# Optimization experiments

Measured on AMD Instinct MI355X. Metric: run time of the kernel, lower is better.

## Reference

```python
import jax, jax.numpy as jnp
import numpy as np

B, S, D_IN, D_H, D_OUT = 8, 4096, 512, 1024, 512


def setup_inputs() -> dict:
    key = jax.random.key(0)
    ks = jax.random.split(key, 7)
    # scale weights by 1/sqrt(fan_in) so activations stay O(1) through the ReLU stack
    return {
        "query": jax.random.normal(ks[0], (B, S, D_IN), dtype=jnp.float32),
        "W0": jax.random.normal(ks[1], (B, D_H, D_IN), dtype=jnp.float32) * (D_IN ** -0.5),
        "b0": jax.random.normal(ks[2], (B, D_H), dtype=jnp.float32) * 0.02,
        "W1": jax.random.normal(ks[3], (B, D_H, D_H), dtype=jnp.float32) * (D_H ** -0.5),
        "b1": jax.random.normal(ks[4], (B, D_H), dtype=jnp.float32) * 0.02,
        "W2": jax.random.normal(ks[5], (B, D_OUT, D_H), dtype=jnp.float32) * (D_H ** -0.5),
        "b2": jax.random.normal(ks[6], (B, D_OUT), dtype=jnp.float32) * 0.02,
    }


def reference(query, W0, b0, W1, b1, W2, b2):
    # Original loops over (seq, batch) issuing F.linear per sample with per-batch
    # weights; this is exactly a batched GEMM over the batch axis.
    # F.linear(x, w, b) = x @ w.T + b, with w[b] of shape [out, in].
    h = jax.nn.relu(jnp.einsum('bsd,bhd->bsh', query, W0) + b0[:, None, :])  # [B,S,H]
    h = jax.nn.relu(jnp.einsum('bsh,bgh->bsg', h, W1) + b1[:, None, :])      # [B,S,H]
    out = jnp.einsum('bsg,bog->bso', h, W2) + b2[:, None, :]                 # [B,S,O]
    return out
```

## Files before the change

kernel.cpp:

```cpp
#include <hip/hip_runtime.h>


typedef _Float16 f16x8 __attribute__((ext_vector_type(8)));
typedef _Float16 f16x4 __attribute__((ext_vector_type(4)));
typedef float    f32x4 __attribute__((ext_vector_type(4)));

__device__ __forceinline__ void stage16(const void* g, void* l) {
    __builtin_amdgcn_global_load_lds(
        (const __attribute__((address_space(1))) unsigned int*)g,
        (__attribute__((address_space(3))) unsigned int*)l,
        16, 0, 0);
}

__device__ __forceinline__ void cast_seg(const float* __restrict__ s,
                                         _Float16* __restrict__ d, int n4) {
    const int stride = gridDim.x * 256;
    for (int i = blockIdx.x * 256 + threadIdx.x; i < n4; i += stride) {
        float4 f = reinterpret_cast<const float4*>(s)[i];
        f16x4 o;
        o[0] = (_Float16)f.x; o[1] = (_Float16)f.y;
        o[2] = (_Float16)f.z; o[3] = (_Float16)f.w;
        reinterpret_cast<f16x4*>(d)[i] = o;
    }
}

__global__ __launch_bounds__(256) void cast_all(
    const float* s0, _Float16* d0, int n0,
    const float* s1, _Float16* d1, int n1,
    const float* s2, _Float16* d2, int n2,
    const float* s3, _Float16* d3, int n3) {
    cast_seg(s0, d0, n0);
    cast_seg(s1, d1, n1);
    cast_seg(s2, d2, n2);
    cast_seg(s3, d3, n3);
}

template <bool RELU, bool OUT_F16>
__global__ __launch_bounds__(512, 2) void gemm_pipe(
    const _Float16* __restrict__ A, const _Float16* __restrict__ W,
    const float* __restrict__ bias, void* __restrict__ Outv,
    int M, int N, int K) {
    constexpr int BM = 256, BN = 256, BK = 32;
    constexpr int DEPTH = 4;
    __shared__ __align__(16) _Float16 As[DEPTH][BM * BK];
    __shared__ __align__(16) _Float16 Bs[DEPTH][BN * BK];

    const int tid  = threadIdx.x;
    const int lane = tid & 63;
    const int rowl = lane & 15;
    const int q8   = (lane >> 4) * 8;
    const int w    = tid >> 6;
    const int wm   = (w >> 2) * 128;
    const int wn   = (w & 3) * 64;

    const int bm = blockIdx.x, bn = blockIdx.y, b = blockIdx.z;

    const int c0 = tid, c1 = tid + 512;
    const int ar0 = c0 >> 2, ak0 = (c0 & 3) * 8;
    const int ar1 = c1 >> 2, ak1 = (c1 & 3) * 8;

    const char* Ab = (const char*)(A + (size_t)b * M * K + (size_t)(bm * BM) * K);
    const char* Wb = (const char*)(W + (size_t)b * N * K + (size_t)(bn * BN) * K);
    size_t aoff0 = ((size_t)ar0 * K + ak0) * 2;
    size_t aoff1 = ((size_t)ar1 * K + ak1) * 2;
    size_t woff0 = ((size_t)ar0 * K + ak0) * 2;
    size_t woff1 = ((size_t)ar1 * K + ak1) * 2;
    constexpr size_t KSTEP = (size_t)BK * 2;

    f32x4 acc[8][4];
#pragma unroll
    for (int mi = 0; mi < 8; ++mi)
#pragma unroll
        for (int ni = 0; ni < 4; ++ni)
            acc[mi][ni] = (f32x4){0.f, 0.f, 0.f, 0.f};

    const int nk = K / BK;

#pragma unroll
    for (int p = 0; p < DEPTH - 1; ++p) {
        if (p < nk) {
            stage16(Ab + aoff0, &As[p][8 * (size_t)c0]);
            stage16(Ab + aoff1, &As[p][8 * (size_t)c1]);
            stage16(Wb + woff0, &Bs[p][8 * (size_t)c0]);
            stage16(Wb + woff1, &Bs[p][8 * (size_t)c1]);
            aoff0 += KSTEP; aoff1 += KSTEP; woff0 += KSTEP; woff1 += KSTEP;
        }
    }
    asm volatile("s_waitcnt vmcnt(8)" ::: "memory");
    __builtin_amdgcn_s_barrier();

    for (int t = 0; t < nk; ++t) {
        const int cur = t & (DEPTH - 1);
        if (t + 3 < nk) {
            const int nxt = (t + 3) & (DEPTH - 1);
            stage16(Ab + aoff0, &As[nxt][8 * (size_t)c0]);
            stage16(Ab + aoff1, &As[nxt][8 * (size_t)c1]);
            stage16(Wb + woff0, &Bs[nxt][8 * (size_t)c0]);
            stage16(Wb + woff1, &Bs[nxt][8 * (size_t)c1]);
            aoff0 += KSTEP; aoff1 += KSTEP; woff0 += KSTEP; woff1 += KSTEP;
        }

        f16x8 af[8], bf[4];
#pragma unroll
        for (int i = 0; i < 8; ++i)
            af[i] = *(const f16x8*)(&As[cur][(wm + i * 16 + rowl) * BK + q8]);
#pragma unroll
        for (int i = 0; i < 4; ++i)
            bf[i] = *(const f16x8*)(&Bs[cur][(wn + i * 16 + rowl) * BK + q8]);

        __builtin_amdgcn_s_setprio(1);
#pragma unroll
        for (int mi = 0; mi < 8; ++mi)
#pragma unroll
            for (int ni = 0; ni < 4; ++ni)
                acc[mi][ni] = __builtin_amdgcn_mfma_f32_16x16x32_f16(
                    af[mi], bf[ni], acc[mi][ni], 0, 0, 0);
        __builtin_amdgcn_s_setprio(0);

        if (t + 1 < nk) {
            if (t + 3 < nk)
                asm volatile("s_waitcnt vmcnt(8)" ::: "memory");
            else if (t + 2 < nk)
                asm volatile("s_waitcnt vmcnt(4)" ::: "memory");
            else
                asm volatile("s_waitcnt vmcnt(0)" ::: "memory");
            __builtin_amdgcn_s_barrier();
        }
    }

    const int q = lane >> 4;
    float bcol[4];
    {
        const float* bp = bias + (size_t)b * N + bn * BN + wn;
#pragma unroll
        for (int ni = 0; ni < 4; ++ni) bcol[ni] = bp[ni * 16 + rowl];
    }
#pragma unroll
    for (int mi = 0; mi < 8; ++mi) {
        const int row0 = bm * BM + wm + mi * 16 + q * 4;
#pragma unroll
        for (int r = 0; r < 4; ++r) {
            const size_t ro = (size_t)b * M * N + (size_t)(row0 + r) * N + bn * BN + wn;
#pragma unroll
            for (int ni = 0; ni < 4; ++ni) {
                float v = acc[mi][ni][r] + bcol[ni];
                if (RELU) v = fmaxf(v, 0.f);
                if (OUT_F16)
                    ((_Float16*)Outv)[ro + ni * 16 + rowl] = (_Float16)v;
                else
                    ((float*)Outv)[ro + ni * 16 + rowl] = v;
            }
        }
    }
}

__device__ __forceinline__ uint4 load8f32(const char* p) {
    const float4* fp = reinterpret_cast<const float4*>(p);
    float4 f0 = fp[0], f1 = fp[1];
    f16x8 o;
    o[0] = (_Float16)f0.x; o[1] = (_Float16)f0.y;
    o[2] = (_Float16)f0.z; o[3] = (_Float16)f0.w;
    o[4] = (_Float16)f1.x; o[5] = (_Float16)f1.y;
    o[6] = (_Float16)f1.z; o[7] = (_Float16)f1.w;
    return __builtin_bit_cast(uint4, o);
}

template <bool A_F16, bool W_F16, bool RELU, bool OUT_F16>
__global__ __launch_bounds__(256) void gemm_bias_act(
    const void* __restrict__ Av, const void* __restrict__ Wv,
    const float* __restrict__ bias, void* __restrict__ Outv,
    int M, int N, int K) {
    constexpr int BM = 128, BN = 128, BK = 32;
    __shared__ __align__(16) _Float16 As[BM * BK];
    __shared__ __align__(16) _Float16 Bs[BN * BK];

    const int tid  = threadIdx.x;
    const int lane = tid & 63;
    const int rowl = lane & 15;
    const int q8   = (lane >> 4) * 8;
    const int wm   = ((tid >> 6) >> 1) * 64;
    const int wn   = ((tid >> 6) & 1) * 64;
    const int bm = blockIdx.x, bn = blockIdx.y, b = blockIdx.z;

    const int c0 = tid, c1 = tid + 256;
    const int ar0 = c0 >> 2, ak0 = (c0 & 3) * 8;
    const int ar1 = c1 >> 2, ak1 = (c1 & 3) * 8;

    constexpr size_t esA = A_F16 ? 2 : 4;
    constexpr size_t esW = W_F16 ? 2 : 4;
    const char* Abase = (const char*)Av;
    const char* Wbase = (const char*)Wv;

    size_t aoff0 = ((size_t)b * M * K + (size_t)(bm * BM + ar0) * K + ak0) * esA;
    size_t aoff1 = ((size_t)b * M * K + (size_t)(bm * BM + ar1) * K + ak1) * esA;
    size_t woff0 = ((size_t)b * N * K + (size_t)(bn * BN + ar0) * K + ak0) * esW;
    size_t woff1 = ((size_t)b * N * K + (size_t)(bn * BN + ar1) * K + ak1) * esW;

    f32x4 acc[4][4];
#pragma unroll
    for (int mi = 0; mi < 4; ++mi)
#pragma unroll
        for (int ni = 0; ni < 4; ++ni)
            acc[mi][ni] = (f32x4){0.f, 0.f, 0.f, 0.f};

    const int nk = K / BK;
    for (int kk = 0; kk < nk; ++kk) {
        uint4 va0, va1, vw0, vw1;
        if (!A_F16) { va0 = load8f32(Abase + aoff0); va1 = load8f32(Abase + aoff1); }
        if (!W_F16) { vw0 = load8f32(Wbase + woff0); vw1 = load8f32(Wbase + woff1); }
        __syncthreads();
        if (A_F16) {
            stage16(Abase + aoff0, As + 8 * (size_t)c0);
            stage16(Abase + aoff1, As + 8 * (size_t)c1);
        } else {
            *(uint4*)(As + ar0 * BK + ak0) = va0;
            *(uint4*)(As + ar1 * BK + ak1) = va1;
        }
        if (W_F16) {
            stage16(Wbase + woff0, Bs + 8 * (size_t)c0);
            stage16(Wbase + woff1, Bs + 8 * (size_t)c1);
        } else {
            *(uint4*)(Bs + ar0 * BK + ak0) = vw0;
            *(uint4*)(Bs + ar1 * BK + ak1) = vw1;
        }
        aoff0 += BK * esA; aoff1 += BK * esA;
        woff0 += BK * esW; woff1 += BK * esW;
        __syncthreads();

        f16x8 af[4], bf[4];
#pragma unroll
        for (int i = 0; i < 4; ++i)
            af[i] = *(const f16x8*)(As + (wm + i * 16 + rowl) * BK + q8);
#pragma unroll
        for (int i = 0; i < 4; ++i)
            bf[i] = *(const f16x8*)(Bs + (wn + i * 16 + rowl) * BK + q8);
#pragma unroll
        for (int mi = 0; mi < 4; ++mi)
#pragma unroll
            for (int ni = 0; ni < 4; ++ni)
                acc[mi][ni] = __builtin_amdgcn_mfma_f32_16x16x32_f16(
                    af[mi], bf[ni], acc[mi][ni], 0, 0, 0);
    }

    const int q = lane >> 4;
    float bcol[4];
    {
        const float* bp = bias + (size_t)b * N + bn * BN + wn;
#pragma unroll
        for (int ni = 0; ni < 4; ++ni) bcol[ni] = bp[ni * 16 + rowl];
    }
#pragma unroll
    for (int mi = 0; mi < 4; ++mi) {
        const int row0 = bm * BM + wm + mi * 16 + q * 4;
#pragma unroll
        for (int r = 0; r < 4; ++r) {
            const size_t ro = (size_t)b * M * N + (size_t)(row0 + r) * N + bn * BN + wn;
#pragma unroll
            for (int ni = 0; ni < 4; ++ni) {
                float v = acc[mi][ni][r] + bcol[ni];
                if (RELU) v = fmaxf(v, 0.f);
                if (OUT_F16)
                    ((_Float16*)Outv)[ro + ni * 16 + rowl] = (_Float16)v;
                else
                    ((float*)Outv)[ro + ni * 16 + rowl] = v;
            }
        }
    }
}

extern "C" void kernel_launch(void* const* d_in, const int* in_sizes, int n_in,
                              void* d_out, int out_size, void* d_ws, size_t ws_size,
                              hipStream_t stream) {
    const int B = 8, S = 4096, DI = 512, DH = 1024, DO = 512;
    const float* query = (const float*)d_in[0];
    const float* W0    = (const float*)d_in[1];
    const float* b0    = (const float*)d_in[2];
    const float* W1    = (const float*)d_in[3];
    const float* b1    = (const float*)d_in[4];
    const float* W2    = (const float*)d_in[5];
    const float* b2    = (const float*)d_in[6];

    char* ws = (char*)d_ws;
    const size_t nH  = (size_t)B * S * DH;
    const size_t nQ  = (size_t)B * S * DI;
    const size_t nW0 = (size_t)B * DH * DI;
    const size_t nW1 = (size_t)B * DH * DH;
    const size_t nW2 = (size_t)B * DO * DH;

    _Float16* h0 = (_Float16*)ws;
    _Float16* h1 = (_Float16*)(ws + nH * 2);
    const size_t off_casts = nH * 4;
    const size_t full_need = off_casts + (nQ + nW0 + nW1 + nW2) * 2;

    if (ws_size >= full_need) {
        _Float16* qf  = (_Float16*)(ws + off_casts);
        _Float16* w0f = qf + nQ;
        _Float16* w1f = w0f + nW0;
        _Float16* w2f = w1f + nW1;
        cast_all<<<dim3(2048), dim3(256), 0, stream>>>(
            query, qf, (int)(nQ / 4), W0, w0f, (int)(nW0 / 4),
            W1, w1f, (int)(nW1 / 4), W2, w2f, (int)(nW2 / 4));
        const dim3 blk(512);
        const dim3 g0(S / 256, DH / 256, B);
        const dim3 g2(S / 256, DO / 256, B);
        gemm_pipe<true,  true ><<<g0, blk, 0, stream>>>(qf, w0f, b0, h0, S, DH, DI);
        gemm_pipe<true,  true ><<<g0, blk, 0, stream>>>(h0, w1f, b1, h1, S, DH, DH);
        gemm_pipe<false, false><<<g2, blk, 0, stream>>>(h1, w2f, b2, d_out, S, DO, DH);
    } else {
        const dim3 blk(256);
        const dim3 g0(S / 128, DH / 128, B);
        const dim3 g2(S / 128, DO / 128, B);
        gemm_bias_act<false, false, true,  true ><<<g0, blk, 0, stream>>>(query, W0, b0, h0, S, DH, DI);
        gemm_bias_act<true,  false, true,  true ><<<g0, blk, 0, stream>>>(h0, W1, b1, h1, S, DH, DH);
        gemm_bias_act<true,  false, false, false><<<g2, blk, 0, stream>>>(h1, W2, b2, d_out, S, DO, DH);
    }
}
```

Measured before the change: 366.2 us.

## Interleave staging loads with MFMA sub-blocks and XOR-swizzle LDS tiles

Restructures the GEMM main loop so each K-step is split into four MFMA sub-blocks, with the global-to-LDS staging loads spread between them and separated by barriers, unrolled by two K-steps. It also XOR-swizzles the 8-element column chunks in both the LDS write addresses and the fragment reads to cut LDS bank conflicts. The goal is better overlap of memory traffic with matrix math and cheaper LDS reads, at the cost of many more barriers per iteration, and it assumes nk is even and at least 4.

```diff
diff --git a/kernel.cpp b/kernel.cpp
--- a/kernel.cpp
+++ b/kernel.cpp
@@ -10,6 +10,15 @@
         (const __attribute__((address_space(1))) unsigned int*)g,
         (__attribute__((address_space(3))) unsigned int*)l,
         16, 0, 0);
+}
+
+template <int CNT> __device__ __forceinline__ void vmwait() {
+    if constexpr (CNT == 8)      asm volatile("s_waitcnt vmcnt(8)" ::: "memory");
+    else if constexpr (CNT == 4) asm volatile("s_waitcnt vmcnt(4)" ::: "memory");
+    else                         asm volatile("s_waitcnt vmcnt(0)" ::: "memory");
+}
+__device__ __forceinline__ void barrier_() {
+    asm volatile("s_barrier" ::: "memory");
 }
 
 __device__ __forceinline__ void cast_seg(const float* __restrict__ s,
@@ -36,7 +45,7 @@
 }
 
 template <bool RELU, bool OUT_F16>
-__global__ __launch_bounds__(512, 2) void gemm_pipe(
+__global__ __launch_bounds__(512, 2) void gemm_pipe8(
     const _Float16* __restrict__ A, const _Float16* __restrict__ W,
     const float* __restrict__ bias, void* __restrict__ Outv,
     int M, int N, int K) {
@@ -48,7 +57,7 @@
     const int tid  = threadIdx.x;
     const int lane = tid & 63;
     const int rowl = lane & 15;
-    const int q8   = (lane >> 4) * 8;
+    const int qswz = (((lane >> 4) ^ ((rowl >> 1) & 3)) * 8);
     const int w    = tid >> 6;
     const int wm   = (w >> 2) * 128;
     const int wn   = (w & 3) * 64;
@@ -56,8 +65,9 @@
     const int bm = blockIdx.x, bn = blockIdx.y, b = blockIdx.z;
 
     const int c0 = tid, c1 = tid + 512;
-    const int ar0 = c0 >> 2, ak0 = (c0 & 3) * 8;
-    const int ar1 = c1 >> 2, ak1 = (c1 & 3) * 8;
+    const int ar0 = c0 >> 2, ar1 = c1 >> 2;
+    const int ak0 = (((c0 & 3) ^ ((ar0 >> 1) & 3)) * 8);
+    const int ak1 = (((c1 & 3) ^ ((ar1 >> 1) & 3)) * 8);
 
     const char* Ab = (const char*)(A + (size_t)b * M * K + (size_t)(bm * BM) * K);
     const char* Wb = (const char*)(W + (size_t)b * N * K + (size_t)(bn * BN) * K);
@@ -75,58 +85,119 @@
             acc[mi][ni] = (f32x4){0.f, 0.f, 0.f, 0.f};
 
     const int nk = K / BK;
+    const int niter = nk / 2;
 
 #pragma unroll
     for (int p = 0; p < DEPTH - 1; ++p) {
-        if (p < nk) {
-            stage16(Ab + aoff0, &As[p][8 * (size_t)c0]);
-            stage16(Ab + aoff1, &As[p][8 * (size_t)c1]);
-            stage16(Wb + woff0, &Bs[p][8 * (size_t)c0]);
-            stage16(Wb + woff1, &Bs[p][8 * (size_t)c1]);
-            aoff0 += KSTEP; aoff1 += KSTEP; woff0 += KSTEP; woff1 += KSTEP;
-        }
-    }
-    asm volatile("s_waitcnt vmcnt(8)" ::: "memory");
-    __builtin_amdgcn_s_barrier();
-
-    for (int t = 0; t < nk; ++t) {
-        const int cur = t & (DEPTH - 1);
-        if (t + 3 < nk) {
-            const int nxt = (t + 3) & (DEPTH - 1);
-            stage16(Ab + aoff0, &As[nxt][8 * (size_t)c0]);
-            stage16(Ab + aoff1, &As[nxt][8 * (size_t)c1]);
-            stage16(Wb + woff0, &Bs[nxt][8 * (size_t)c0]);
-            stage16(Wb + woff1, &Bs[nxt][8 * (size_t)c1]);
-            aoff0 += KSTEP; aoff1 += KSTEP; woff0 += KSTEP; woff1 += KSTEP;
-        }
-
-        f16x8 af[8], bf[4];
-#pragma unroll
-        for (int i = 0; i < 8; ++i)
-            af[i] = *(const f16x8*)(&As[cur][(wm + i * 16 + rowl) * BK + q8]);
-#pragma unroll
-        for (int i = 0; i < 4; ++i)
-            bf[i] = *(const f16x8*)(&Bs[cur][(wn + i * 16 + rowl) * BK + q8]);
-
-        __builtin_amdgcn_s_setprio(1);
-#pragma unroll
-        for (int mi = 0; mi < 8; ++mi)
-#pragma unroll
-            for (int ni = 0; ni < 4; ++ni)
-                acc[mi][ni] = __builtin_amdgcn_mfma_f32_16x16x32_f16(
-                    af[mi], bf[ni], acc[mi][ni], 0, 0, 0);
-        __builtin_amdgcn_s_setprio(0);
-
-        if (t + 1 < nk) {
-            if (t + 3 < nk)
-                asm volatile("s_waitcnt vmcnt(8)" ::: "memory");
-            else if (t + 2 < nk)
-                asm volatile("s_waitcnt vmcnt(4)" ::: "memory");
-            else
-                asm volatile("s_waitcnt vmcnt(0)" ::: "memory");
-            __builtin_amdgcn_s_barrier();
-        }
-    }
+        stage16(Ab + aoff0, &As[p][8 * (size_t)c0]);
+        stage16(Ab + aoff1, &As[p][8 * (size_t)c1]);
+        stage16(Wb + woff0, &Bs[p][8 * (size_t)c0]);
+        stage16(Wb + woff1, &Bs[p][8 * (size_t)c1]);
+        aoff0 += KSTEP; aoff1 += KSTEP; woff0 += KSTEP; woff1 += KSTEP;
+    }
+    vmwait<8>();
+    barrier_();
+
+#define BFLOAD(SS)                                                            \
+    bf[0] = *(const f16x8*)(&Bs[SS][(wn +  0 + rowl) * BK + qswz]);           \
+    bf[1] = *(const f16x8*)(&Bs[SS][(wn + 16 + rowl) * BK + qswz]);           \
+    bf[2] = *(const f16x8*)(&Bs[SS][(wn + 32 + rowl) * BK + qswz]);           \
+    bf[3] = *(const f16x8*)(&Bs[SS][(wn + 48 + rowl) * BK + qswz]);
+
+#define LDA2(SS, MI)                                                          \
+    f16x8 a0 = *(const f16x8*)(&As[SS][(wm + (MI)*16 + rowl) * BK + qswz]);   \
+    f16x8 a1 = *(const f16x8*)(&As[SS][(wm + (MI)*16 + 16 + rowl) * BK + qswz]);
+
+#define MFMA8(MI)                                                             \
+    __builtin_amdgcn_s_setprio(1);                                            \
+    acc[MI][0]   = __builtin_amdgcn_mfma_f32_16x16x32_f16(a0, bf[0], acc[MI][0],   0, 0, 0); \
+    acc[MI][1]   = __builtin_amdgcn_mfma_f32_16x16x32_f16(a0, bf[1], acc[MI][1],   0, 0, 0); \
+    acc[MI][2]   = __builtin_amdgcn_mfma_f32_16x16x32_f16(a0, bf[2], acc[MI][2],   0, 0, 0); \
+    acc[MI][3]   = __builtin_amdgcn_mfma_f32_16x16x32_f16(a0, bf[3], acc[MI][3],   0, 0, 0); \
+    acc[MI+1][0] = __builtin_amdgcn_mfma_f32_16x16x32_f16(a1, bf[0], acc[MI+1][0], 0, 0, 0); \
+    acc[MI+1][1] = __builtin_amdgcn_mfma_f32_16x16x32_f16(a1, bf[1], acc[MI+1][1], 0, 0, 0); \
+    acc[MI+1][2] = __builtin_amdgcn_mfma_f32_16x16x32_f16(a1, bf[2], acc[MI+1][2], 0, 0, 0); \
+    acc[MI+1][3] = __builtin_amdgcn_mfma_f32_16x16x32_f16(a1, bf[3], acc[MI+1][3], 0, 0, 0); \
+    __builtin_amdgcn_s_setprio(0);
+
+    for (int i = 0; i < niter; ++i) {
+        const int t0 = 2 * i;
+        const int s0 = t0 & 3, s1 = (t0 + 1) & 3;
+        const int sA = (t0 + 3) & 3;
+        const int sB = s0;
+        const bool stg03 = (t0 + 3 < nk);
+        const bool stg47 = (t0 + 4 < nk);
+
+        f16x8 bf[4];
+
+        {
+            BFLOAD(s0);
+            LDA2(s0, 0);
+            if (stg03) stage16(Ab + aoff0, &As[sA][8 * (size_t)c0]);
+            barrier_();
+            MFMA8(0);
+            barrier_();
+        }
+        {
+            LDA2(s0, 2);
+            if (stg03) stage16(Ab + aoff1, &As[sA][8 * (size_t)c1]);
+            barrier_();
+            MFMA8(2);
+            barrier_();
+        }
+        {
+            LDA2(s0, 4);
+            if (stg03) stage16(Wb + woff0, &Bs[sA][8 * (size_t)c0]);
+            barrier_();
+            MFMA8(4);
+            barrier_();
+        }
+        {
+            LDA2(s0, 6);
+            if (stg03) stage16(Wb + woff1, &Bs[sA][8 * (size_t)c1]);
+            barrier_();
+            MFMA8(6);
+            if (i + 1 < niter) vmwait<8>(); else vmwait<0>();
+            barrier_();
+        }
+        aoff0 += KSTEP; aoff1 += KSTEP; woff0 += KSTEP; woff1 += KSTEP;
+
+        {
+            BFLOAD(s1);
+            LDA2(s1, 0);
+            if (stg47) stage16(Ab + aoff0, &As[sB][8 * (size_t)c0]);
+            barrier_();
+            MFMA8(0);
+            barrier_();
+        }
+        {
+            LDA2(s1, 2);
+            if (stg47) stage16(Ab + aoff1, &As[sB][8 * (size_t)c1]);
+            barrier_();
+            MFMA8(2);
+            barrier_();
+        }
+        {
+            LDA2(s1, 4);
+            if (stg47) stage16(Wb + woff0, &Bs[sB][8 * (size_t)c0]);
+            barrier_();
+            MFMA8(4);
+            barrier_();
+        }
+        {
+            LDA2(s1, 6);
+            if (stg47) stage16(Wb + woff1, &Bs[sB][8 * (size_t)c1]);
+            barrier_();
+            MFMA8(6);
+            if (i + 2 < niter)      vmwait<8>();
+            else if (i + 1 < niter) vmwait<4>();
+            barrier_();
+        }
+        aoff0 += KSTEP; aoff1 += KSTEP; woff0 += KSTEP; woff1 += KSTEP;
+    }
+#undef BFLOAD
+#undef LDA2
+#undef MFMA8
 
     const int q = lane >> 4;
     float bcol[4];
@@ -303,9 +374,9 @@
         const dim3 blk(512);
         const dim3 g0(S / 256, DH / 256, B);
         const dim3 g2(S / 256, DO / 256, B);
-        gemm_pipe<true,  true ><<<g0, blk, 0, stream>>>(qf, w0f, b0, h0, S, DH, DI);
-        gemm_pipe<true,  true ><<<g0, blk, 0, stream>>>(h0, w1f, b1, h1, S, DH, DH);
-        gemm_pipe<false, false><<<g2, blk, 0, stream>>>(h1, w2f, b2, d_out, S, DO, DH);
+        gemm_pipe8<true,  true ><<<g0, blk, 0, stream>>>(qf, w0f, b0, h0, S, DH, DI);
+        gemm_pipe8<true,  true ><<<g0, blk, 0, stream>>>(h0, w1f, b1, h1, S, DH, DH);
+        gemm_pipe8<false, false><<<g2, blk, 0, stream>>>(h1, w2f, b2, d_out, S, DO, DH);
     } else {
         const dim3 blk(256);
         const dim3 g0(S / 128, DH / 128, B);
```

Result: faster. 337.8 us (-7.8%).

## Double-buffer LDS fragment reads, swizzle LDS layout, and remap blocks for XCD locality

Applied to the files above, without the earlier changes.

The main loop is restructured and unrolled by two, with two register fragment sets. LDS reads for the next k-step are issued before the MFMAs of the current one, so LDS latency overlaps with matrix math, and one barrier per step remains. The LDS layout gets an XOR swizzle on the 8-element k-chunk to cut bank conflicts. The grid is flattened to 1D and block IDs are remapped so that consecutive tiles land on the same XCD, which should improve L2 reuse. The extra fragment registers raise register pressure, and the loop assumes nk is even.

```diff
diff --git a/kernel.cpp b/kernel.cpp
--- a/kernel.cpp
+++ b/kernel.cpp
@@ -10,6 +10,16 @@
         (const __attribute__((address_space(1))) unsigned int*)g,
         (__attribute__((address_space(3))) unsigned int*)l,
         16, 0, 0);
+}
+
+template <int CNT> __device__ __forceinline__ void vmwait() {
+    if constexpr (CNT == 8)      asm volatile("s_waitcnt vmcnt(8)");
+    else if constexpr (CNT == 4) asm volatile("s_waitcnt vmcnt(4)");
+    else                         asm volatile("s_waitcnt vmcnt(0)");
+}
+__device__ __forceinline__ void barrier_() {
+    __builtin_amdgcn_sched_barrier(0);
+    __builtin_amdgcn_s_barrier();
 }
 
 __device__ __forceinline__ void cast_seg(const float* __restrict__ s,
@@ -36,7 +46,7 @@
 }
 
 template <bool RELU, bool OUT_F16>
-__global__ __launch_bounds__(512, 2) void gemm_pipe(
+__global__ __launch_bounds__(512, 2) void gemm_olap(
     const _Float16* __restrict__ A, const _Float16* __restrict__ W,
     const float* __restrict__ bias, void* __restrict__ Outv,
     int M, int N, int K) {
@@ -48,16 +58,25 @@
     const int tid  = threadIdx.x;
     const int lane = tid & 63;
     const int rowl = lane & 15;
-    const int q8   = (lane >> 4) * 8;
+    const int qswz = (((lane >> 4) ^ ((rowl >> 1) & 3)) * 8);
     const int w    = tid >> 6;
     const int wm   = (w >> 2) * 128;
     const int wn   = (w & 3) * 64;
 
-    const int bm = blockIdx.x, bn = blockIdx.y, b = blockIdx.z;
+    const int nwg = gridDim.x;
+    const int cpx = nwg >> 3;
+    const int sw  = (blockIdx.x & 7) * cpx + (blockIdx.x >> 3);
+    const int MB  = M >> 8;
+    const int NB  = N >> 8;
+    const int bm  = sw % MB;
+    const int rr  = sw / MB;
+    const int bn  = rr % NB;
+    const int b   = rr / NB;
 
     const int c0 = tid, c1 = tid + 512;
-    const int ar0 = c0 >> 2, ak0 = (c0 & 3) * 8;
-    const int ar1 = c1 >> 2, ak1 = (c1 & 3) * 8;
+    const int ar0 = c0 >> 2, ar1 = c1 >> 2;
+    const int ak0 = (((c0 & 3) ^ ((ar0 >> 1) & 3)) * 8);
+    const int ak1 = (((c1 & 3) ^ ((ar1 >> 1) & 3)) * 8);
 
     const char* Ab = (const char*)(A + (size_t)b * M * K + (size_t)(bm * BM) * K);
     const char* Wb = (const char*)(W + (size_t)b * N * K + (size_t)(bn * BN) * K);
@@ -78,55 +97,64 @@
 
 #pragma unroll
     for (int p = 0; p < DEPTH - 1; ++p) {
-        if (p < nk) {
-            stage16(Ab + aoff0, &As[p][8 * (size_t)c0]);
-            stage16(Ab + aoff1, &As[p][8 * (size_t)c1]);
-            stage16(Wb + woff0, &Bs[p][8 * (size_t)c0]);
-            stage16(Wb + woff1, &Bs[p][8 * (size_t)c1]);
-            aoff0 += KSTEP; aoff1 += KSTEP; woff0 += KSTEP; woff1 += KSTEP;
-        }
-    }
-    asm volatile("s_waitcnt vmcnt(8)" ::: "memory");
-    __builtin_amdgcn_s_barrier();
-
-    for (int t = 0; t < nk; ++t) {
-        const int cur = t & (DEPTH - 1);
-        if (t + 3 < nk) {
-            const int nxt = (t + 3) & (DEPTH - 1);
-            stage16(Ab + aoff0, &As[nxt][8 * (size_t)c0]);
-            stage16(Ab + aoff1, &As[nxt][8 * (size_t)c1]);
-            stage16(Wb + woff0, &Bs[nxt][8 * (size_t)c0]);
-            stage16(Wb + woff1, &Bs[nxt][8 * (size_t)c1]);
-            aoff0 += KSTEP; aoff1 += KSTEP; woff0 += KSTEP; woff1 += KSTEP;
-        }
-
-        f16x8 af[8], bf[4];
-#pragma unroll
-        for (int i = 0; i < 8; ++i)
-            af[i] = *(const f16x8*)(&As[cur][(wm + i * 16 + rowl) * BK + q8]);
-#pragma unroll
-        for (int i = 0; i < 4; ++i)
-            bf[i] = *(const f16x8*)(&Bs[cur][(wn + i * 16 + rowl) * BK + q8]);
-
-        __builtin_amdgcn_s_setprio(1);
-#pragma unroll
-        for (int mi = 0; mi < 8; ++mi)
-#pragma unroll
-            for (int ni = 0; ni < 4; ++ni)
-                acc[mi][ni] = __builtin_amdgcn_mfma_f32_16x16x32_f16(
-                    af[mi], bf[ni], acc[mi][ni], 0, 0, 0);
-        __builtin_amdgcn_s_setprio(0);
-
-        if (t + 1 < nk) {
-            if (t + 3 < nk)
-                asm volatile("s_waitcnt vmcnt(8)" ::: "memory");
-            else if (t + 2 < nk)
-                asm volatile("s_waitcnt vmcnt(4)" ::: "memory");
-            else
-                asm volatile("s_waitcnt vmcnt(0)" ::: "memory");
-            __builtin_amdgcn_s_barrier();
-        }
-    }
+        stage16(Ab + aoff0, &As[p][8 * (size_t)c0]);
+        stage16(Ab + aoff1, &As[p][8 * (size_t)c1]);
+        stage16(Wb + woff0, &Bs[p][8 * (size_t)c0]);
+        stage16(Wb + woff1, &Bs[p][8 * (size_t)c1]);
+        aoff0 += KSTEP; aoff1 += KSTEP; woff0 += KSTEP; woff1 += KSTEP;
+    }
+    vmwait<8>();
+    barrier_();
+
+    f16x8 afA[8], bfA[4], afB[8], bfB[4];
+
+#define READS(AF, BF, SS)                                                     \
+    BF[0] = *(const f16x8*)(&Bs[SS][(wn +  0 + rowl) * BK + qswz]);           \
+    BF[1] = *(const f16x8*)(&Bs[SS][(wn + 16 + rowl) * BK + qswz]);           \
+    BF[2] = *(const f16x8*)(&Bs[SS][(wn + 32 + rowl) * BK + qswz]);           \
+    BF[3] = *(const f16x8*)(&Bs[SS][(wn + 48 + rowl) * BK + qswz]);           \
+    _Pragma("unroll")                                                         \
+    for (int mi = 0; mi < 8; ++mi)                                            \
+        AF[mi] = *(const f16x8*)(&As[SS][(wm + mi * 16 + rowl) * BK + qswz]);
+
+#define STAGE(SS)                                                             \
+    stage16(Ab + aoff0, &As[SS][8 * (size_t)c0]);                             \
+    stage16(Ab + aoff1, &As[SS][8 * (size_t)c1]);                             \
+    stage16(Wb + woff0, &Bs[SS][8 * (size_t)c0]);                             \
+    stage16(Wb + woff1, &Bs[SS][8 * (size_t)c1]);                             \
+    aoff0 += KSTEP; aoff1 += KSTEP; woff0 += KSTEP; woff1 += KSTEP;
+
+#define MFMA32(AF, BF)                                                        \
+    __builtin_amdgcn_s_setprio(1);                                            \
+    _Pragma("unroll")                                                         \
+    for (int mi = 0; mi < 8; ++mi) {                                          \
+        acc[mi][0] = __builtin_amdgcn_mfma_f32_16x16x32_f16(AF[mi], BF[0], acc[mi][0], 0, 0, 0); \
+        acc[mi][1] = __builtin_amdgcn_mfma_f32_16x16x32_f16(AF[mi], BF[1], acc[mi][1], 0, 0, 0); \
+        acc[mi][2] = __builtin_amdgcn_mfma_f32_16x16x32_f16(AF[mi], BF[2], acc[mi][2], 0, 0, 0); \
+        acc[mi][3] = __builtin_amdgcn_mfma_f32_16x16x32_f16(AF[mi], BF[3], acc[mi][3], 0, 0, 0); \
+    }                                                                         \
+    __builtin_amdgcn_s_setprio(0);
+
+    READS(afA, bfA, 0);
+
+    for (int i = 0; i < nk / 2; ++i) {
+        const int t0 = 2 * i, t1 = t0 + 1;
+
+        if (t0 + 2 < nk) vmwait<4>(); else vmwait<0>();
+        barrier_();
+        if (t0 + 3 < nk) { STAGE((t0 + 3) & 3); }
+        READS(afB, bfB, t1 & 3);
+        MFMA32(afA, bfA);
+
+        if (t1 + 2 < nk) vmwait<4>(); else vmwait<0>();
+        barrier_();
+        if (t1 + 3 < nk) { STAGE((t1 + 3) & 3); }
+        if (t1 + 1 < nk) { READS(afA, bfA, (t1 + 1) & 3); }
+        MFMA32(afB, bfB);
+    }
+#undef READS
+#undef STAGE
+#undef MFMA32
 
     const int q = lane >> 4;
     float bcol[4];
@@ -301,11 +329,11 @@
             query, qf, (int)(nQ / 4), W0, w0f, (int)(nW0 / 4),
             W1, w1f, (int)(nW1 / 4), W2, w2f, (int)(nW2 / 4));
         const dim3 blk(512);
-        const dim3 g0(S / 256, DH / 256, B);
-        const dim3 g2(S / 256, DO / 256, B);
-        gemm_pipe<true,  true ><<<g0, blk, 0, stream>>>(qf, w0f, b0, h0, S, DH, DI);
-        gemm_pipe<true,  true ><<<g0, blk, 0, stream>>>(h0, w1f, b1, h1, S, DH, DH);
-        gemm_pipe<false, false><<<g2, blk, 0, stream>>>(h1, w2f, b2, d_out, S, DO, DH);
+        const dim3 g0(dim3((S / 256) * (DH / 256) * B));
+        const dim3 g2(dim3((S / 256) * (DO / 256) * B));
+        gemm_olap<true,  true ><<<g0, blk, 0, stream>>>(qf, w0f, b0, h0, S, DH, DI);
+        gemm_olap<true,  true ><<<g0, blk, 0, stream>>>(h0, w1f, b1, h1, S, DH, DH);
+        gemm_olap<false, false><<<g2, blk, 0, stream>>>(h1, w2f, b2, d_out, S, DO, DH);
     } else {
         const dim3 blk(256);
         const dim3 g0(S / 128, DH / 128, B);
```

Measured after the change: 346.6 us. 5.4% less time.
